# Optimization experiments

Hardware: AMD Instinct MI355X
Metric: run time of the kernel (lower is better)

## Reference

```python
import jax, jax.numpy as jnp
import numpy as np

K_NEIGHBORS = 6
LN_EPS = 1e-5


def _layernorm(h, g, b):
    m = h.mean(-1, keepdims=True)
    v = h.var(-1, keepdims=True)
    return (h - m) / jnp.sqrt(v + LN_EPS) * g + b


def _mlp(h, w0, b0, w1, b1):
    return jax.nn.relu(h @ w0 + b0) @ w1 + b1


def _learn_adj(x, Wp, bp):
    # EfficientGraphStructureLearner: cosine-sim topk graph, symmetrized, row-normalized
    h = x @ Wp + bp
    nrm = jnp.linalg.norm(h, axis=1, keepdims=True)
    h = h / jnp.maximum(nrm, 1e-12)
    S = h @ h.T                                  # [N, N]
    vals, idx = jax.lax.top_k(S, K_NEIGHBORS + 1)  # col 0 is self (diag == 1)
    N = x.shape[0]
    rows = jnp.arange(N)[:, None]
    adj = jnp.zeros_like(S).at[rows, idx[:, 1:]].set(vals[:, 1:])
    adj = (adj + adj.T) * 0.5
    adj = adj / (adj.sum(1, keepdims=True) + 1e-8)
    return adj


def _gcn(h, adj, W, b):
    # StandardGraphConv: D^-1/2 (A+I) D^-1/2 @ (h W) + b (diag matmuls as row/col scaling)
    A = adj + jnp.eye(adj.shape[0], dtype=adj.dtype)
    d = jnp.maximum(A.sum(1), 1e-12) ** -0.5
    norm_adj = d[:, None] * A * d[None, :]
    return norm_adj @ (h @ W) + b


def setup_inputs() -> dict:
    key = jax.random.key(0)
    ks = iter(jax.random.split(key, 40))
    N, D, H, O, HP = 8192, 20, 32, 128, 16
    f = lambda *s: jax.random.normal(next(ks), s, dtype=jnp.float32) * 0.1
    inp = {
        'x': jax.random.normal(next(ks), (N, D), dtype=jnp.float32),
        'Wp': f(D, HP), 'bp': jnp.zeros((HP,), jnp.float32),
        'gw0': f(D, H), 'gb0': jnp.zeros((H,), jnp.float32),
        'gw1': f(H, H), 'gb1': jnp.zeros((H,), jnp.float32),
        'gw2': f(H, O), 'gb2': jnp.zeros((O,), jnp.float32),
        'lg0': jnp.ones((H,), jnp.float32), 'lb0': jnp.zeros((H,), jnp.float32),
        'lg1': jnp.ones((H,), jnp.float32), 'lb1': jnp.zeros((H,), jnp.float32),
        'lg2': jnp.ones((O,), jnp.float32), 'lb2': jnp.zeros((O,), jnp.float32),
        'riw0': f(D, H), 'rib0': jnp.zeros((H,), jnp.float32),
        'riw1': f(H, H), 'rib1': jnp.zeros((H,), jnp.float32),
        'rhw0': f(H, H), 'rhb0': jnp.zeros((H,), jnp.float32),
        'rhw1': f(H, H), 'rhb1': jnp.zeros((H,), jnp.float32),
        'row0': f(H, O), 'rob0': jnp.zeros((O,), jnp.float32),
        'row1': f(O, O), 'rob1': jnp.zeros((O,), jnp.float32),
    }
    return inp


def reference(x, Wp, bp, gw0, gb0, gw1, gb1, gw2, gb2,
              lg0, lb0, lg1, lb1, lg2, lb2,
              riw0, rib0, riw1, rib1,
              rhw0, rhb0, rhw1, rhb1,
              row0, rob0, row1, rob1):
    adj = _learn_adj(x, Wp, bp)
    gcns = [(gw0, gb0, lg0, lb0), (gw1, gb1, lg1, lb1), (gw2, gb2, lg2, lb2)]
    skips = [(riw0, rib0, riw1, rib1), (rhw0, rhb0, rhw1, rhb1), (row0, rob0, row1, rob1)]
    h = x
    for i, ((W, b, g, bt), sk) in enumerate(zip(gcns, skips)):
        h_new = jax.nn.relu(_layernorm(_gcn(h, adj, W, b), g, bt))
        h = h_new + _mlp(h, *sk)
        # dropout is identity in eval mode
    return h
```

## Files before the change

### kernel.cpp

```cpp
#include <hip/hip_runtime.h>

constexpr int D_IN = 20;
constexpr int HP   = 16;
constexpr int K    = 6;
constexpr int SAMP = 512;
constexpr int NC   = 8;
constexpr int CAPC = 192;
constexpr int CIN  = 128;
constexpr float MARGIN = 0.02f;

typedef __attribute__((ext_vector_type(8))) short bf16x8;
typedef __attribute__((ext_vector_type(4))) float f32x4;

__device__ __forceinline__ float dot16_seq(const float4* q, const float4* c) {
  float s = 0.f;
#pragma unroll
  for (int m = 0; m < 4; ++m) {
    s = fmaf(q[m].x, c[m].x, s);
    s = fmaf(q[m].y, c[m].y, s);
    s = fmaf(q[m].z, c[m].z, s);
    s = fmaf(q[m].w, c[m].w, s);
  }
  return s;
}

__device__ __forceinline__ short f2bf(float f) {
  unsigned u = __float_as_uint(f);
  unsigned r = (u + 0x7fffu + ((u >> 16) & 1u)) >> 16;
  return (short)r;
}

__device__ __forceinline__ float dinv_of(float own, float ins) {
  float rs = 0.5f * (own + ins);
  float rn = 1.f / (rs + 1e-8f);
  return rsqrtf(fmaxf(1.f + rs * rn, 1e-12f));
}

__global__ void k_proj(const float* __restrict__ x, const float* __restrict__ Wp,
                       const float* __restrict__ bp, const float* __restrict__ gw0,
                       float* __restrict__ hn, short* __restrict__ hnb,
                       float* __restrict__ XW0,
                       float* __restrict__ insum, int* __restrict__ indeg, int N) {
  int i = blockIdx.x * blockDim.x + threadIdx.x;
  if (i >= N) return;
  insum[i] = 0.f; indeg[i] = 0;
  float xr[D_IN];
#pragma unroll
  for (int d = 0; d < D_IN; ++d) xr[d] = x[i*D_IN + d];
  float hv[HP];
  float nrm2 = 0.f;
#pragma unroll
  for (int h = 0; h < HP; ++h) {
    float a = bp[h];
#pragma unroll
    for (int d = 0; d < D_IN; ++d) a += xr[d] * Wp[d*HP + h];
    hv[h] = a;
    nrm2 += a * a;
  }
  float inv = 1.f / fmaxf(sqrtf(nrm2), 1e-12f);
#pragma unroll
  for (int h = 0; h < HP; ++h) {
    float v = hv[h] * inv;
    hn[i*HP + h] = v;
    hnb[(size_t)i*32 + h] = f2bf(v);
  }
#pragma unroll
  for (int h = 0; h < HP; ++h) hnb[(size_t)i*32 + 16 + h] = 0;
#pragma unroll
  for (int oc = 0; oc < 32; ++oc) {
    float a = 0.f;
#pragma unroll
    for (int d = 0; d < D_IN; ++d) a += xr[d] * gw0[d*32 + oc];
    XW0[(size_t)i*32 + oc] = a;
  }
}

struct Top6 { float v0,v1,v2,v3,v4,v5; int i0,i1,i2,i3,i4,i5; };

__device__ __forceinline__ void t6_init(Top6& t) {
  t.v0=t.v1=t.v2=t.v3=t.v4=t.v5=-1e30f;
  t.i0=t.i1=t.i2=t.i3=t.i4=t.i5=-1;
}

#define T6_SWAP(a,b,ia,ib) { float tv=a; a=b; b=tv; int ti=ia; ia=ib; ib=ti; }

__device__ __forceinline__ void t6_insert(Top6& t, float s, int c) {
  if (s > t.v5) {
    t.v5 = s; t.i5 = c;
    if (t.v5 > t.v4) { T6_SWAP(t.v4, t.v5, t.i4, t.i5); }
    if (t.v4 > t.v3) { T6_SWAP(t.v3, t.v4, t.i3, t.i4); }
    if (t.v3 > t.v2) { T6_SWAP(t.v2, t.v3, t.i2, t.i3); }
    if (t.v2 > t.v1) { T6_SWAP(t.v1, t.v2, t.i1, t.i2); }
    if (t.v1 > t.v0) { T6_SWAP(t.v0, t.v1, t.i0, t.i1); }
  }
}

__device__ __forceinline__ void t6_best(const Top6& t, float& cv, int& ci) {
  cv = t.v0; ci = t.i0;
  if (t.v1 > cv || (t.v1 == cv && (unsigned)t.i1 < (unsigned)ci)) { cv = t.v1; ci = t.i1; }
  if (t.v2 > cv || (t.v2 == cv && (unsigned)t.i2 < (unsigned)ci)) { cv = t.v2; ci = t.i2; }
  if (t.v3 > cv || (t.v3 == cv && (unsigned)t.i3 < (unsigned)ci)) { cv = t.v3; ci = t.i3; }
  if (t.v4 > cv || (t.v4 == cv && (unsigned)t.i4 < (unsigned)ci)) { cv = t.v4; ci = t.i4; }
  if (t.v5 > cv || (t.v5 == cv && (unsigned)t.i5 < (unsigned)ci)) { cv = t.v5; ci = t.i5; }
}

__device__ __forceinline__ void t6_consume(Top6& t, int mi) {
  if (t.i0 == mi) t.v0 = -1e30f;
  if (t.i1 == mi) t.v1 = -1e30f;
  if (t.i2 == mi) t.v2 = -1e30f;
  if (t.i3 == mi) t.v3 = -1e30f;
  if (t.i4 == mi) t.v4 = -1e30f;
  if (t.i5 == mi) t.v5 = -1e30f;
}

__global__ __launch_bounds__(256) void k_thresh(const float* __restrict__ hn,
                                                float* __restrict__ tau, int N) {
  int wave = threadIdx.x >> 6, lane = threadIdx.x & 63;
  int row = blockIdx.x * 4 + wave;
  const float4* hn4 = (const float4*)hn;
  float4 q[4];
#pragma unroll
  for (int m = 0; m < 4; ++m) q[m] = hn4[(size_t)row*4 + m];
  Top6 t; t6_init(t);
#pragma unroll
  for (int k = 0; k < SAMP/64; ++k) {
    int c = lane + 64*k;
    if (c != row) {
      float4 cv[4];
#pragma unroll
      for (int m = 0; m < 4; ++m) cv[m] = hn4[(size_t)c*4 + m];
      float s = dot16_seq(q, cv);
      t6_insert(t, s, c);
    }
  }
  float last = -1e30f;
  for (int sel = 0; sel < K; ++sel) {
    float cv; int ci;
    t6_best(t, cv, ci);
    float mv = cv; int mi = ci;
#pragma unroll
    for (int m = 1; m < 64; m <<= 1) {
      float ov = __shfl_xor(mv, m);
      int   oi = __shfl_xor(mi, m);
      if (ov > mv || (ov == mv && (unsigned)oi < (unsigned)mi)) { mv = ov; mi = oi; }
    }
    t6_consume(t, mi);
    last = mv;
  }
  if (lane == 0) tau[row] = last;
}

__global__ __launch_bounds__(256) void k_scan2(
    const short* __restrict__ hnb, const float* __restrict__ tau,
    int* __restrict__ cnt, unsigned short* __restrict__ buf, int N) {
  __shared__ int cntl[16];
  int rb = blockIdx.x / NC;
  int jc = blockIdx.x % NC;
  int wave = threadIdx.x >> 6, lane = threadIdx.x & 63;
  int r0 = rb * 16;
  int half = lane >> 4;
  int l16  = lane & 15;

  if (threadIdx.x < 16) cntl[threadIdx.x] = 0;
  __syncthreads();

  bf16x8 a = *(const bf16x8*)(hnb + (size_t)(r0 + l16)*32 + half*8);
  float4 t4 = *(const float4*)(tau + r0 + half*4);
  float tm0 = t4.x - MARGIN, tm1 = t4.y - MARGIN,
        tm2 = t4.z - MARGIN, tm3 = t4.w - MARGIN;
  f32x4 zero = {0.f, 0.f, 0.f, 0.f};

  const int SPANW = N / NC / 4;
  int jb0 = jc * (N / NC) + wave * SPANW;

#define APPB(R, COND)                                                        \
  {                                                                          \
    unsigned long long mr = __ballot(COND);                                  \
    if (l16 == 0) {                                                          \
      unsigned mask = (unsigned)(mr >> (16*half)) & 0xFFFFu;                 \
      if (mask) {                                                            \
        int row = r0 + half*4 + (R);                                         \
        int pos = atomicAdd(&cntl[4*half + (R)], __popc(mask));              \
        unsigned mm = mask;                                                  \
        while (mm) {                                                         \
          int bx = __ffs(mm) - 1; mm &= mm - 1;                              \
          if (pos < CAPC)                                                    \
            buf[((size_t)row*NC + jc)*CAPC + pos] = (unsigned short)(jb + bx); \
          ++pos;                                                             \
        }                                                                    \
      }                                                                      \
    }                                                                        \
  }

#pragma unroll 4
  for (int jt = 0; jt < SPANW; jt += 16) {
    int jb = jb0 + jt;
    bf16x8 b = *(const bf16x8*)(hnb + (size_t)(jb + l16)*32 + half*8);
    f32x4 d = __builtin_amdgcn_mfma_f32_16x16x32_bf16(a, b, zero, 0, 0, 0);
    bool h0 = d[0] >= tm0, h1 = d[1] >= tm1, h2 = d[2] >= tm2, h3 = d[3] >= tm3;
    if (__any(h0 | h1 | h2 | h3)) {
      APPB(0, h0) APPB(1, h1) APPB(2, h2) APPB(3, h3)
    }
  }
#undef APPB

  __syncthreads();
  if (threadIdx.x < 16)
    cnt[(size_t)(r0 + threadIdx.x)*NC + jc] = min(cntl[threadIdx.x], CAPC);
}

__global__ __launch_bounds__(256) void k_final(
    const float* __restrict__ hn, const unsigned short* __restrict__ buf,
    const int* __restrict__ cnt,
    float* __restrict__ evals, int* __restrict__ eidx,
    float* __restrict__ ownsum, float* insum, int* indeg,
    unsigned short* __restrict__ incol, float* __restrict__ inval, int N) {
  int wave = threadIdx.x >> 6, lane = threadIdx.x & 63;
  int row = blockIdx.x * 4 + wave;
  const float4* hn4 = (const float4*)hn;
  float4 q[4];
#pragma unroll
  for (int m = 0; m < 4; ++m) q[m] = hn4[(size_t)row*4 + m];

  int cbase = row * NC;
  int cl = (lane < NC) ? cnt[cbase + lane] : 0;
  int c0 = __shfl(cl, 0), c1 = __shfl(cl, 1), c2 = __shfl(cl, 2), c3 = __shfl(cl, 3),
      c4 = __shfl(cl, 4), c5 = __shfl(cl, 5), c6 = __shfl(cl, 6), c7 = __shfl(cl, 7);
  int p1 = c0, p2 = p1 + c1, p3 = p2 + c2, p4 = p3 + c3,
      p5 = p4 + c4, p6 = p5 + c5, p7 = p6 + c6, T = p7 + c7;

  Top6 t; t6_init(t);
  for (int e = lane; e < T; e += 64) {
    int s, off;
    if (e < p4) {
      if (e < p2) { if (e < p1) { s = 0; off = e; } else { s = 1; off = e - p1; } }
      else        { if (e < p3) { s = 2; off = e - p2; } else { s = 3; off = e - p3; } }
    } else {
      if (e < p6) { if (e < p5) { s = 4; off = e - p4; } else { s = 5; off = e - p5; } }
      else        { if (e < p7) { s = 6; off = e - p6; } else { s = 7; off = e - p7; } }
    }
    int j = buf[((size_t)cbase + s)*CAPC + off];
    if (j != row) {
      float4 cv[4];
#pragma unroll
      for (int m = 0; m < 4; ++m) cv[m] = hn4[(size_t)j*4 + m];
      float sc = dot16_seq(q, cv);
      t6_insert(t, sc, j);
    }
  }
  float osum = 0.f;
  for (int sel = 0; sel < K; ++sel) {
    float cv; int ci;
    t6_best(t, cv, ci);
    float mv = cv; int mi = ci;
#pragma unroll
    for (int m = 1; m < 64; m <<= 1) {
      float ov = __shfl_xor(mv, m);
      int   oi = __shfl_xor(mi, m);
      if (ov > mv || (ov == mv && (unsigned)oi < (unsigned)mi)) { mv = ov; mi = oi; }
    }
    t6_consume(t, mi);
    if (lane == 0) {
      evals[row*K + sel] = mv;
      eidx [row*K + sel] = mi;
      osum += mv;
      atomicAdd(&insum[mi], mv);
      int pos = atomicAdd(&indeg[mi], 1);
      if (pos < CIN) {
        incol[(size_t)mi*CIN + pos] = (unsigned short)row;
        inval[(size_t)mi*CIN + pos] = mv;
      }
    }
  }
  if (lane == 0) ownsum[row] = osum;
}

template<int DIN, int NEXTD>
__global__ __launch_bounds__(256) void k_gpost32(
    const float* __restrict__ XWsrc,
    const int* __restrict__ eidx, const float* __restrict__ evals,
    const unsigned short* __restrict__ incol, const float* __restrict__ inval,
    const int* __restrict__ indeg,
    const float* __restrict__ ownsum, const float* __restrict__ insum,
    const float* __restrict__ gb, const float* __restrict__ lg, const float* __restrict__ lb,
    const float* __restrict__ hprev,
    const float* __restrict__ w0, const float* __restrict__ b0,
    const float* __restrict__ w1, const float* __restrict__ b1,
    const float* __restrict__ Wnext, float* __restrict__ XWnext,
    float* __restrict__ outp, int N) {
  __shared__ float hid[4][2][32];
  int tid = threadIdx.x;
  int lane = tid & 63, wslot = tid >> 6;
  int sub = lane >> 5, ol = lane & 31;
  int row = (blockIdx.x * 4 + wslot) * 2 + sub;

  float rs_i = 0.5f * (ownsum[row] + insum[row]);
  float rn_i = 1.f / (rs_i + 1e-8f);
  float di_i = rsqrtf(fmaxf(1.f + rs_i * rn_i, 1e-12f));
  float cc = 0.5f * di_i * rn_i;
  float acc = (di_i * di_i) * XWsrc[(size_t)row*32 + ol];
#pragma unroll
  for (int t = 0; t < K; ++t) {
    int j = eidx[row*K + t]; float v = evals[row*K + t];
    float dj = dinv_of(ownsum[j], insum[j]);
    acc = fmaf(cc * v * dj, XWsrc[(size_t)j*32 + ol], acc);
  }
  int ne = min(indeg[row], CIN);
  for (int e = 0; e < ne; ++e) {
    int j = incol[(size_t)row*CIN + e]; float v = inval[(size_t)row*CIN + e];
    float dj = dinv_of(ownsum[j], insum[j]);
    acc = fmaf(cc * v * dj, XWsrc[(size_t)j*32 + ol], acc);
  }
  float u0 = acc + gb[ol];
  float s = u0;
#pragma unroll
  for (int m = 1; m < 32; m <<= 1) s += __shfl_xor(s, m);
  float mean = s * (1.f/32.f);
  float d0 = u0 - mean;
  float vs = d0*d0;
#pragma unroll
  for (int m = 1; m < 32; m <<= 1) vs += __shfl_xor(vs, m);
  float rstd = rsqrtf(vs * (1.f/32.f) + 1e-5f);
  float t0 = fmaxf(d0*rstd*lg[ol] + lb[ol], 0.f);

  float hp[DIN];
#pragma unroll
  for (int d = 0; d < DIN; ++d) hp[d] = hprev[(size_t)row*DIN + d];
  float a = b0[ol];
#pragma unroll
  for (int d = 0; d < DIN; ++d) a = fmaf(hp[d], w0[d*32 + ol], a);
  hid[wslot][sub][ol] = fmaxf(a, 0.f);
  float o = b1[ol];
#pragma unroll
  for (int h = 0; h < 32; ++h) o = fmaf(hid[wslot][sub][h], w1[h*32 + ol], o);
  float hv = t0 + o;
  outp[(size_t)row*32 + ol] = hv;

  hid[wslot][sub][ol] = hv;
#pragma unroll
  for (int k2 = 0; k2 < NEXTD/32; ++k2) {
    int oc = ol + 32*k2;
    float acc2 = 0.f;
#pragma unroll
    for (int d = 0; d < 32; ++d)
      acc2 = fmaf(hid[wslot][sub][d], Wnext[d*NEXTD + oc], acc2);
    XWnext[(size_t)row*NEXTD + oc] = acc2;
  }
}

__global__ __launch_bounds__(256) void k_gpost128(
    const float* __restrict__ XW,
    const int* __restrict__ eidx, const float* __restrict__ evals,
    const unsigned short* __restrict__ incol, const float* __restrict__ inval,
    const int* __restrict__ indeg,
    const float* __restrict__ ownsum, const float* __restrict__ insum,
    const float* __restrict__ b, const float* __restrict__ g, const float* __restrict__ bt,
    const float* __restrict__ hprev,
    const float* __restrict__ w0, const float* __restrict__ b0,
    const float* __restrict__ w1, const float* __restrict__ b1,
    float* __restrict__ out, int N) {
  __shared__ float hid_s[4][128];
  int wslot = threadIdx.x >> 6;
  int row   = (blockIdx.x * blockDim.x + threadIdx.x) >> 6;
  int lane  = threadIdx.x & 63;
  int o0 = lane, o1 = lane + 64;

  float rs_i = 0.5f * (ownsum[row] + insum[row]);
  float rn_i = 1.f / (rs_i + 1e-8f);
  float di_i = rsqrtf(fmaxf(1.f + rs_i * rn_i, 1e-12f));
  float cc = 0.5f * di_i * rn_i;
  float sc = di_i * di_i;
  float acc0 = sc * XW[(size_t)row*128 + o0];
  float acc1 = sc * XW[(size_t)row*128 + o1];
#pragma unroll
  for (int t = 0; t < K; ++t) {
    int j = eidx[row*K + t]; float v = evals[row*K + t];
    float dj = dinv_of(ownsum[j], insum[j]);
    float cf = cc * v * dj;
    acc0 = fmaf(cf, XW[(size_t)j*128 + o0], acc0);
    acc1 = fmaf(cf, XW[(size_t)j*128 + o1], acc1);
  }
  int ne = min(indeg[row], CIN);
  for (int e = 0; e < ne; ++e) {
    int j = incol[(size_t)row*CIN + e]; float v = inval[(size_t)row*CIN + e];
    float dj = dinv_of(ownsum[j], insum[j]);
    float cf = cc * v * dj;
    acc0 = fmaf(cf, XW[(size_t)j*128 + o0], acc0);
    acc1 = fmaf(cf, XW[(size_t)j*128 + o1], acc1);
  }
  float u0 = acc0 + b[o0];
  float u1 = acc1 + b[o1];

  float s = u0 + u1;
#pragma unroll
  for (int m = 1; m < 64; m <<= 1) s += __shfl_xor(s, m);
  float mean = s * (1.f/128.f);
  float d0 = u0 - mean, d1 = u1 - mean;
  float vs = d0*d0 + d1*d1;
#pragma unroll
  for (int m = 1; m < 64; m <<= 1) vs += __shfl_xor(vs, m);
  float rstd = rsqrtf(vs * (1.f/128.f) + 1e-5f);
  float t0 = fmaxf(d0*rstd*g[o0] + bt[o0], 0.f);
  float t1 = fmaxf(d1*rstd*g[o1] + bt[o1], 0.f);

  float hp[32];
#pragma unroll
  for (int d = 0; d < 32; ++d) hp[d] = hprev[(size_t)row*32 + d];
  {
    float a = b0[o0];
#pragma unroll
    for (int d = 0; d < 32; ++d) a = fmaf(hp[d], w0[d*128 + o0], a);
    hid_s[wslot][o0] = fmaxf(a, 0.f);
    float a1 = b0[o1];
#pragma unroll
    for (int d = 0; d < 32; ++d) a1 = fmaf(hp[d], w0[d*128 + o1], a1);
    hid_s[wslot][o1] = fmaxf(a1, 0.f);
  }
  __syncthreads();
  {
    float a = b1[o0];
#pragma unroll 4
    for (int h = 0; h < 128; ++h) a = fmaf(hid_s[wslot][h], w1[h*128 + o0], a);
    out[(size_t)row*128 + o0] = t0 + a;
    float a1 = b1[o1];
#pragma unroll 4
    for (int h = 0; h < 128; ++h) a1 = fmaf(hid_s[wslot][h], w1[h*128 + o1], a1);
    out[(size_t)row*128 + o1] = t1 + a1;
  }
}

extern "C" void kernel_launch(void* const* d_in, const int* in_sizes, int n_in,
                              void* d_out, int out_size, void* d_ws, size_t ws_size,
                              hipStream_t stream) {
  const float* x    = (const float*)d_in[0];
  const float* Wp   = (const float*)d_in[1];
  const float* bp   = (const float*)d_in[2];
  const float* gw0  = (const float*)d_in[3];
  const float* gb0  = (const float*)d_in[4];
  const float* gw1  = (const float*)d_in[5];
  const float* gb1  = (const float*)d_in[6];
  const float* gw2  = (const float*)d_in[7];
  const float* gb2  = (const float*)d_in[8];
  const float* lg0  = (const float*)d_in[9];
  const float* lb0  = (const float*)d_in[10];
  const float* lg1  = (const float*)d_in[11];
  const float* lb1  = (const float*)d_in[12];
  const float* lg2  = (const float*)d_in[13];
  const float* lb2  = (const float*)d_in[14];
  const float* riw0 = (const float*)d_in[15];
  const float* rib0 = (const float*)d_in[16];
  const float* riw1 = (const float*)d_in[17];
  const float* rib1 = (const float*)d_in[18];
  const float* rhw0 = (const float*)d_in[19];
  const float* rhb0 = (const float*)d_in[20];
  const float* rhw1 = (const float*)d_in[21];
  const float* rhb1 = (const float*)d_in[22];
  const float* row0 = (const float*)d_in[23];
  const float* rob0 = (const float*)d_in[24];
  const float* row1 = (const float*)d_in[25];
  const float* rob1 = (const float*)d_in[26];
  int N = in_sizes[0] / D_IN;
  float* out = (float*)d_out;

  char* ws = (char*)d_ws;
  size_t off = 0;
  auto alloc = [&](size_t bytes) -> void* {
    void* p = ws + off;
    off += (bytes + 255) & ~(size_t)255;
    return p;
  };
  float* hn      = (float*)alloc((size_t)N * HP * 4);
  float* evals   = (float*)alloc((size_t)N * K * 4);
  int*   eidx    = (int*)  alloc((size_t)N * K * 4);
  float* ownsum  = (float*)alloc((size_t)N * 4);
  float* insum   = (float*)alloc((size_t)N * 4);
  int*   indeg   = (int*)  alloc((size_t)N * 4);
  float* XWa     = (float*)alloc((size_t)N * 128 * 4);
  float* XWb     = (float*)alloc((size_t)N * 32 * 4);
  float* h1      = (float*)alloc((size_t)N * 32 * 4);
  float* h2      = (float*)alloc((size_t)N * 32 * 4);
  float* tau     = (float*)alloc((size_t)N * 4);
  int*   cnt     = (int*)  alloc((size_t)N * NC * 4);
  unsigned short* buf = (unsigned short*)alloc((size_t)N * NC * CAPC * 2);
  short* hnb     = (short*)alloc((size_t)N * 32 * 2);
  unsigned short* incol = (unsigned short*)alloc((size_t)N * CIN * 2);
  float* inval   = (float*)alloc((size_t)N * CIN * 4);
  (void)ws_size; (void)n_in; (void)out_size;

  const int B = 256;
  hipLaunchKernelGGL(k_proj, dim3((N + B - 1) / B), dim3(B), 0, stream,
                     x, Wp, bp, gw0, hn, hnb, XWa, insum, indeg, N);
  hipLaunchKernelGGL(k_thresh, dim3(N / 4), dim3(B), 0, stream, hn, tau, N);
  hipLaunchKernelGGL(k_scan2, dim3((N / 16) * NC), dim3(B), 0, stream, hnb, tau, cnt, buf, N);
  hipLaunchKernelGGL(k_final, dim3(N / 4), dim3(B), 0, stream,
                     hn, buf, cnt, evals, eidx, ownsum, insum, indeg, incol, inval, N);

  hipLaunchKernelGGL((k_gpost32<20, 32>), dim3(N / 8), dim3(B), 0, stream,
                     XWa, eidx, evals, incol, inval, indeg, ownsum, insum,
                     gb0, lg0, lb0, x, riw0, rib0, riw1, rib1, gw1, XWb, h1, N);
  hipLaunchKernelGGL((k_gpost32<32, 128>), dim3(N / 8), dim3(B), 0, stream,
                     XWb, eidx, evals, incol, inval, indeg, ownsum, insum,
                     gb1, lg1, lb1, h1, rhw0, rhb0, rhw1, rhb1, gw2, XWa, h2, N);
  hipLaunchKernelGGL(k_gpost128, dim3(N / 4), dim3(B), 0, stream,
                     XWa, eidx, evals, incol, inval, indeg, ownsum, insum,
                     gb2, lg2, lb2, h2, row0, rob0, row1, rob1, out, N);
}
```

Measured before the change: 164.8 us.

## Cache normalized edge coefficients in first GCN pass and reuse in later layers

The first aggregation kernel now writes the per-edge normalized coefficients and the self-loop coefficient to workspace. The later two layers read these back instead of recomputing degree normalization from ownsum and insum gathers. The gather loops are unrolled by four with independent loads, the small MLP dot products use multiple accumulators, and the 128-wide kernel uses float2 vector loads and stores. The cost is extra global writes in layer one and extra coefficient reads later, in exchange for removing dependent random gathers and the associated arithmetic.

```diff
diff --git a/kernel.cpp b/kernel.cpp
--- a/kernel.cpp
+++ b/kernel.cpp
@@ -275,13 +275,14 @@
   if (lane == 0) ownsum[row] = osum;
 }
 
-template<int DIN, int NEXTD>
+template<int DIN, int NEXTD, bool FIRST>
 __global__ __launch_bounds__(256) void k_gpost32(
     const float* __restrict__ XWsrc,
     const int* __restrict__ eidx, const float* __restrict__ evals,
     const unsigned short* __restrict__ incol, const float* __restrict__ inval,
     const int* __restrict__ indeg,
     const float* __restrict__ ownsum, const float* __restrict__ insum,
+    float* __restrict__ selfc, float* __restrict__ coefK, float* __restrict__ coefIN,
     const float* __restrict__ gb, const float* __restrict__ lg, const float* __restrict__ lb,
     const float* __restrict__ hprev,
     const float* __restrict__ w0, const float* __restrict__ b0,
@@ -294,22 +295,53 @@
   int sub = lane >> 5, ol = lane & 31;
   int row = (blockIdx.x * 4 + wslot) * 2 + sub;
 
-  float rs_i = 0.5f * (ownsum[row] + insum[row]);
-  float rn_i = 1.f / (rs_i + 1e-8f);
-  float di_i = rsqrtf(fmaxf(1.f + rs_i * rn_i, 1e-12f));
-  float cc = 0.5f * di_i * rn_i;
-  float acc = (di_i * di_i) * XWsrc[(size_t)row*32 + ol];
-#pragma unroll
-  for (int t = 0; t < K; ++t) {
-    int j = eidx[row*K + t]; float v = evals[row*K + t];
-    float dj = dinv_of(ownsum[j], insum[j]);
-    acc = fmaf(cc * v * dj, XWsrc[(size_t)j*32 + ol], acc);
-  }
+  float acc;
   int ne = min(indeg[row], CIN);
-  for (int e = 0; e < ne; ++e) {
-    int j = incol[(size_t)row*CIN + e]; float v = inval[(size_t)row*CIN + e];
-    float dj = dinv_of(ownsum[j], insum[j]);
-    acc = fmaf(cc * v * dj, XWsrc[(size_t)j*32 + ol], acc);
+  if constexpr (FIRST) {
+    float rs_i = 0.5f * (ownsum[row] + insum[row]);
+    float rn_i = 1.f / (rs_i + 1e-8f);
+    float di_i = rsqrtf(fmaxf(1.f + rs_i * rn_i, 1e-12f));
+    float cc = 0.5f * di_i * rn_i;
+    float sc = di_i * di_i;
+    if (ol == 0) selfc[row] = sc;
+    acc = sc * XWsrc[(size_t)row*32 + ol];
+#pragma unroll
+    for (int t = 0; t < K; ++t) {
+      int j = eidx[row*K + t]; float v = evals[row*K + t];
+      float dj = dinv_of(ownsum[j], insum[j]);
+      float cf = cc * v * dj;
+      if (ol == 0) coefK[row*K + t] = cf;
+      acc = fmaf(cf, XWsrc[(size_t)j*32 + ol], acc);
+    }
+    for (int e = 0; e < ne; ++e) {
+      int j = incol[(size_t)row*CIN + e]; float v = inval[(size_t)row*CIN + e];
+      float dj = dinv_of(ownsum[j], insum[j]);
+      float cf = cc * v * dj;
+      if (ol == 0) coefIN[(size_t)row*CIN + e] = cf;
+      acc = fmaf(cf, XWsrc[(size_t)j*32 + ol], acc);
+    }
+  } else {
+    acc = selfc[row] * XWsrc[(size_t)row*32 + ol];
+#pragma unroll
+    for (int t = 0; t < K; ++t) {
+      int j = eidx[row*K + t]; float cf = coefK[row*K + t];
+      acc = fmaf(cf, XWsrc[(size_t)j*32 + ol], acc);
+    }
+    const unsigned short* icp = incol + (size_t)row*CIN;
+    const float* cfp = coefIN + (size_t)row*CIN;
+    for (int e0 = 0; e0 < ne; e0 += 4) {
+      int j0 = icp[e0];                          float cf0 = cfp[e0];
+      int b1v = e0+1 < ne, b2v = e0+2 < ne, b3v = e0+3 < ne;
+      int j1 = b1v ? icp[e0+1] : j0;             float cf1 = b1v ? cfp[e0+1] : 0.f;
+      int j2 = b2v ? icp[e0+2] : j0;             float cf2 = b2v ? cfp[e0+2] : 0.f;
+      int j3 = b3v ? icp[e0+3] : j0;             float cf3 = b3v ? cfp[e0+3] : 0.f;
+      float v0 = XWsrc[(size_t)j0*32 + ol], v1 = XWsrc[(size_t)j1*32 + ol],
+            v2 = XWsrc[(size_t)j2*32 + ol], v3 = XWsrc[(size_t)j3*32 + ol];
+      acc = fmaf(cf0, v0, acc);
+      acc = fmaf(cf1, v1, acc);
+      acc = fmaf(cf2, v2, acc);
+      acc = fmaf(cf3, v3, acc);
+    }
   }
   float u0 = acc + gb[ol];
   float s = u0;
@@ -330,30 +362,38 @@
 #pragma unroll
   for (int d = 0; d < DIN; ++d) a = fmaf(hp[d], w0[d*32 + ol], a);
   hid[wslot][sub][ol] = fmaxf(a, 0.f);
-  float o = b1[ol];
-#pragma unroll
-  for (int h = 0; h < 32; ++h) o = fmaf(hid[wslot][sub][h], w1[h*32 + ol], o);
-  float hv = t0 + o;
+  float r0 = 0.f, r1 = 0.f, r2 = 0.f, r3 = 0.f;
+#pragma unroll
+  for (int h = 0; h < 32; h += 4) {
+    r0 = fmaf(hid[wslot][sub][h+0], w1[(h+0)*32 + ol], r0);
+    r1 = fmaf(hid[wslot][sub][h+1], w1[(h+1)*32 + ol], r1);
+    r2 = fmaf(hid[wslot][sub][h+2], w1[(h+2)*32 + ol], r2);
+    r3 = fmaf(hid[wslot][sub][h+3], w1[(h+3)*32 + ol], r3);
+  }
+  float hv = t0 + b1[ol] + ((r0 + r1) + (r2 + r3));
   outp[(size_t)row*32 + ol] = hv;
 
   hid[wslot][sub][ol] = hv;
 #pragma unroll
   for (int k2 = 0; k2 < NEXTD/32; ++k2) {
     int oc = ol + 32*k2;
-    float acc2 = 0.f;
-#pragma unroll
-    for (int d = 0; d < 32; ++d)
-      acc2 = fmaf(hid[wslot][sub][d], Wnext[d*NEXTD + oc], acc2);
-    XWnext[(size_t)row*NEXTD + oc] = acc2;
+    float e0 = 0.f, e1 = 0.f, e2 = 0.f, e3 = 0.f;
+#pragma unroll
+    for (int d = 0; d < 32; d += 4) {
+      e0 = fmaf(hid[wslot][sub][d+0], Wnext[(d+0)*NEXTD + oc], e0);
+      e1 = fmaf(hid[wslot][sub][d+1], Wnext[(d+1)*NEXTD + oc], e1);
+      e2 = fmaf(hid[wslot][sub][d+2], Wnext[(d+2)*NEXTD + oc], e2);
+      e3 = fmaf(hid[wslot][sub][d+3], Wnext[(d+3)*NEXTD + oc], e3);
+    }
+    XWnext[(size_t)row*NEXTD + oc] = (e0 + e1) + (e2 + e3);
   }
 }
 
 __global__ __launch_bounds__(256) void k_gpost128(
     const float* __restrict__ XW,
-    const int* __restrict__ eidx, const float* __restrict__ evals,
-    const unsigned short* __restrict__ incol, const float* __restrict__ inval,
-    const int* __restrict__ indeg,
-    const float* __restrict__ ownsum, const float* __restrict__ insum,
+    const int* __restrict__ eidx, const float* __restrict__ coefK,
+    const unsigned short* __restrict__ incol, const float* __restrict__ coefIN,
+    const int* __restrict__ indeg, const float* __restrict__ selfc,
     const float* __restrict__ b, const float* __restrict__ g, const float* __restrict__ bt,
     const float* __restrict__ hprev,
     const float* __restrict__ w0, const float* __restrict__ b0,
@@ -363,33 +403,35 @@
   int wslot = threadIdx.x >> 6;
   int row   = (blockIdx.x * blockDim.x + threadIdx.x) >> 6;
   int lane  = threadIdx.x & 63;
-  int o0 = lane, o1 = lane + 64;
-
-  float rs_i = 0.5f * (ownsum[row] + insum[row]);
-  float rn_i = 1.f / (rs_i + 1e-8f);
-  float di_i = rsqrtf(fmaxf(1.f + rs_i * rn_i, 1e-12f));
-  float cc = 0.5f * di_i * rn_i;
-  float sc = di_i * di_i;
-  float acc0 = sc * XW[(size_t)row*128 + o0];
-  float acc1 = sc * XW[(size_t)row*128 + o1];
+  const float2* XW2 = (const float2*)XW;
+
+  float sc = selfc[row];
+  float2 xs = XW2[(size_t)row*64 + lane];
+  float acc0 = sc * xs.x, acc1 = sc * xs.y;
 #pragma unroll
   for (int t = 0; t < K; ++t) {
-    int j = eidx[row*K + t]; float v = evals[row*K + t];
-    float dj = dinv_of(ownsum[j], insum[j]);
-    float cf = cc * v * dj;
-    acc0 = fmaf(cf, XW[(size_t)j*128 + o0], acc0);
-    acc1 = fmaf(cf, XW[(size_t)j*128 + o1], acc1);
+    int j = eidx[row*K + t]; float cf = coefK[row*K + t];
+    float2 v = XW2[(size_t)j*64 + lane];
+    acc0 = fmaf(cf, v.x, acc0); acc1 = fmaf(cf, v.y, acc1);
   }
   int ne = min(indeg[row], CIN);
-  for (int e = 0; e < ne; ++e) {
-    int j = incol[(size_t)row*CIN + e]; float v = inval[(size_t)row*CIN + e];
-    float dj = dinv_of(ownsum[j], insum[j]);
-    float cf = cc * v * dj;
-    acc0 = fmaf(cf, XW[(size_t)j*128 + o0], acc0);
-    acc1 = fmaf(cf, XW[(size_t)j*128 + o1], acc1);
-  }
-  float u0 = acc0 + b[o0];
-  float u1 = acc1 + b[o1];
+  const unsigned short* icp = incol + (size_t)row*CIN;
+  const float* cfp = coefIN + (size_t)row*CIN;
+  for (int e0 = 0; e0 < ne; e0 += 4) {
+    int j0 = icp[e0];                      float c0 = cfp[e0];
+    int b1v = e0+1 < ne, b2v = e0+2 < ne, b3v = e0+3 < ne;
+    int j1 = b1v ? icp[e0+1] : j0;         float c1 = b1v ? cfp[e0+1] : 0.f;
+    int j2 = b2v ? icp[e0+2] : j0;         float c2 = b2v ? cfp[e0+2] : 0.f;
+    int j3 = b3v ? icp[e0+3] : j0;         float c3 = b3v ? cfp[e0+3] : 0.f;
+    float2 v0 = XW2[(size_t)j0*64 + lane], v1 = XW2[(size_t)j1*64 + lane],
+           v2 = XW2[(size_t)j2*64 + lane], v3 = XW2[(size_t)j3*64 + lane];
+    acc0 = fmaf(c0, v0.x, acc0); acc1 = fmaf(c0, v0.y, acc1);
+    acc0 = fmaf(c1, v1.x, acc0); acc1 = fmaf(c1, v1.y, acc1);
+    acc0 = fmaf(c2, v2.x, acc0); acc1 = fmaf(c2, v2.y, acc1);
+    acc0 = fmaf(c3, v3.x, acc0); acc1 = fmaf(c3, v3.y, acc1);
+  }
+  float2 bv = ((const float2*)b)[lane];
+  float u0 = acc0 + bv.x, u1 = acc1 + bv.y;
 
   float s = u0 + u1;
 #pragma unroll
@@ -400,33 +442,44 @@
 #pragma unroll
   for (int m = 1; m < 64; m <<= 1) vs += __shfl_xor(vs, m);
   float rstd = rsqrtf(vs * (1.f/128.f) + 1e-5f);
-  float t0 = fmaxf(d0*rstd*g[o0] + bt[o0], 0.f);
-  float t1 = fmaxf(d1*rstd*g[o1] + bt[o1], 0.f);
+  float2 gv = ((const float2*)g)[lane], btv = ((const float2*)bt)[lane];
+  float t0 = fmaxf(d0*rstd*gv.x + btv.x, 0.f);
+  float t1 = fmaxf(d1*rstd*gv.y + btv.y, 0.f);
 
   float hp[32];
 #pragma unroll
   for (int d = 0; d < 32; ++d) hp[d] = hprev[(size_t)row*32 + d];
-  {
-    float a = b0[o0];
-#pragma unroll
-    for (int d = 0; d < 32; ++d) a = fmaf(hp[d], w0[d*128 + o0], a);
-    hid_s[wslot][o0] = fmaxf(a, 0.f);
-    float a1 = b0[o1];
-#pragma unroll
-    for (int d = 0; d < 32; ++d) a1 = fmaf(hp[d], w0[d*128 + o1], a1);
-    hid_s[wslot][o1] = fmaxf(a1, 0.f);
-  }
+  const float2* w02 = (const float2*)w0;
+  float2 b0v = ((const float2*)b0)[lane];
+  float a0 = b0v.x, a1 = b0v.y;
+#pragma unroll
+  for (int d = 0; d < 32; ++d) {
+    float2 wv = w02[(size_t)d*64 + lane];
+    a0 = fmaf(hp[d], wv.x, a0);
+    a1 = fmaf(hp[d], wv.y, a1);
+  }
+  ((float2*)hid_s[wslot])[lane] = make_float2(fmaxf(a0, 0.f), fmaxf(a1, 0.f));
   __syncthreads();
-  {
-    float a = b1[o0];
-#pragma unroll 4
-    for (int h = 0; h < 128; ++h) a = fmaf(hid_s[wslot][h], w1[h*128 + o0], a);
-    out[(size_t)row*128 + o0] = t0 + a;
-    float a1 = b1[o1];
-#pragma unroll 4
-    for (int h = 0; h < 128; ++h) a1 = fmaf(hid_s[wslot][h], w1[h*128 + o1], a1);
-    out[(size_t)row*128 + o1] = t1 + a1;
-  }
+
+  const float2* w12 = (const float2*)w1;
+  float r0=0.f, r1=0.f, r2=0.f, r3=0.f, q0=0.f, q1=0.f, q2=0.f, q3=0.f;
+#pragma unroll
+  for (int h = 0; h < 128; h += 4) {
+    float h0 = hid_s[wslot][h+0], h1 = hid_s[wslot][h+1],
+          h2 = hid_s[wslot][h+2], h3 = hid_s[wslot][h+3];
+    float2 wa = w12[(size_t)(h+0)*64 + lane];
+    float2 wb = w12[(size_t)(h+1)*64 + lane];
+    float2 wc = w12[(size_t)(h+2)*64 + lane];
+    float2 wd = w12[(size_t)(h+3)*64 + lane];
+    r0 = fmaf(h0, wa.x, r0); q0 = fmaf(h0, wa.y, q0);
+    r1 = fmaf(h1, wb.x, r1); q1 = fmaf(h1, wb.y, q1);
+    r2 = fmaf(h2, wc.x, r2); q2 = fmaf(h2, wc.y, q2);
+    r3 = fmaf(h3, wd.x, r3); q3 = fmaf(h3, wd.y, q3);
+  }
+  float2 b1v = ((const float2*)b1)[lane];
+  float ox = t0 + b1v.x + ((r0 + r1) + (r2 + r3));
+  float oy = t1 + b1v.y + ((q0 + q1) + (q2 + q3));
+  ((float2*)out)[(size_t)row*64 + lane] = make_float2(ox, oy);
 }
 
 extern "C" void kernel_launch(void* const* d_in, const int* in_sizes, int n_in,
@@ -485,6 +538,9 @@
   short* hnb     = (short*)alloc((size_t)N * 32 * 2);
   unsigned short* incol = (unsigned short*)alloc((size_t)N * CIN * 2);
   float* inval   = (float*)alloc((size_t)N * CIN * 4);
+  float* selfc   = (float*)alloc((size_t)N * 4);
+  float* coefK   = (float*)alloc((size_t)N * K * 4);
+  float* coefIN  = (float*)alloc((size_t)N * CIN * 4);
   (void)ws_size; (void)n_in; (void)out_size;
 
   const int B = 256;
@@ -495,13 +551,15 @@
   hipLaunchKernelGGL(k_final, dim3(N / 4), dim3(B), 0, stream,
                      hn, buf, cnt, evals, eidx, ownsum, insum, indeg, incol, inval, N);
 
-  hipLaunchKernelGGL((k_gpost32<20, 32>), dim3(N / 8), dim3(B), 0, stream,
+  hipLaunchKernelGGL((k_gpost32<20, 32, true>), dim3(N / 8), dim3(B), 0, stream,
                      XWa, eidx, evals, incol, inval, indeg, ownsum, insum,
+                     selfc, coefK, coefIN,
                      gb0, lg0, lb0, x, riw0, rib0, riw1, rib1, gw1, XWb, h1, N);
-  hipLaunchKernelGGL((k_gpost32<32, 128>), dim3(N / 8), dim3(B), 0, stream,
+  hipLaunchKernelGGL((k_gpost32<32, 128, false>), dim3(N / 8), dim3(B), 0, stream,
                      XWb, eidx, evals, incol, inval, indeg, ownsum, insum,
+                     selfc, coefK, coefIN,
                      gb1, lg1, lb1, h1, rhw0, rhb0, rhw1, rhb1, gw2, XWa, h2, N);
   hipLaunchKernelGGL(k_gpost128, dim3(N / 4), dim3(B), 0, stream,
-                     XWa, eidx, evals, incol, inval, indeg, ownsum, insum,
+                     XWa, eidx, coefK, incol, coefIN, indeg, selfc,
                      gb2, lg2, lb2, h2, row0, rob0, row1, rob1, out, N);
 }
```

New measurement: 173.7 us (median of 2 runs). 5.4% more time.
